# Kernel tuning notes

Hardware: AMD Instinct MI355X
Metric: run time of the kernel (lower is better)

The kernel has to match this reference:

```python
import jax, jax.numpy as jnp
import numpy as np

COV_EMB = 32
N_HEAD = 2
FACTOR_TCL = 2   # TemporalConvolutionalLayer factor (default 2)
FACTOR_MLP = 1   # MLP factor passed from MultiAttention init
EPS = 1e-5


def _conv1d_causal(x, w, b):
    # x: [N, C, T], w: [O, C, 3]; torch pads 2 both sides then slices [..., :-2],
    # equivalent to left-pad 2 only -> output length T.
    y = jax.lax.conv_general_dilated(x, w, window_strides=(1,), padding=[(2, 0)],
                                     dimension_numbers=('NCH', 'OIH', 'NCH'))
    return y + b[None, :, None]


def _tcl(x, w_conv, b_conv, w_proj, b_proj):
    # TemporalConvolutionalLayer: x [..., T, C] -> [..., T, C]
    shp = x.shape
    T, C = shp[-2], shp[-1]
    x2 = x.reshape(-1, T, C).transpose(0, 2, 1)              # [N, C, T]
    h = jax.nn.gelu(_conv1d_causal(x2, w_conv, b_conv), approximate=False)
    h = h.transpose(0, 2, 1)                                  # [N, T, 2C]
    out = h @ w_proj.T + b_proj                               # [N, T, C]
    return out.reshape(*shp[:-1], C)


def _layernorm(x, w):
    mu = jnp.mean(x, axis=-1, keepdims=True)
    var = jnp.var(x, axis=-1, keepdims=True)
    return (x - mu) * jax.lax.rsqrt(var + EPS) * w


def setup_inputs() -> dict:
    key = jax.random.key(0)
    ks = jax.random.split(key, 20)
    C = COV_EMB
    C2 = FACTOR_TCL * C
    s = 0.02
    inp = {
        'causal_decoder': jax.random.normal(ks[0], (8, 4, 1024, C), jnp.float32),
        'past_kv': jax.random.normal(ks[1], (8, 1024, C), jnp.float32),
    }
    def tcl_params(i):
        return (jax.random.normal(ks[i], (C2, C, 3), jnp.float32) * s,
                jnp.zeros((C2,), jnp.float32),
                jax.random.normal(ks[i + 1], (C, C2), jnp.float32) * s,
                jnp.zeros((C,), jnp.float32))
    inp['wq_conv'], inp['bq_conv'], inp['wq_proj'], inp['bq_proj'] = tcl_params(2)
    inp['wk_conv'], inp['bk_conv'], inp['wk_proj'], inp['bk_proj'] = tcl_params(4)
    inp['wv_conv'], inp['bv_conv'], inp['wv_proj'], inp['bv_proj'] = tcl_params(6)
    inp['w_cproj'] = jax.random.normal(ks[8], (C, C), jnp.float32) * s   # bias=False
    inp['ln_w'] = jnp.ones((C,), jnp.float32)                            # bias=False
    inp['w_fc'] = jax.random.normal(ks[9], (FACTOR_MLP * C, C), jnp.float32) * s   # bias=False
    inp['w_mlp_proj'] = jax.random.normal(ks[10], (C, FACTOR_MLP * C), jnp.float32) * s
    return inp


def reference(causal_decoder, past_kv,
              wq_conv, bq_conv, wq_proj, bq_proj,
              wk_conv, bk_conv, wk_proj, bk_proj,
              wv_conv, bv_conv, wv_proj, bv_proj,
              w_cproj, ln_w, w_fc, w_mlp_proj):
    B, F, T, C = causal_decoder.shape
    nh, hd = N_HEAD, C // N_HEAD

    q = _tcl(causal_decoder, wq_conv, bq_conv, wq_proj, bq_proj)   # [B,F,T,C]
    k = _tcl(past_kv, wk_conv, bk_conv, wk_proj, bk_proj)          # [B,S,C]
    v = _tcl(past_kv, wv_conv, bv_conv, wv_proj, bv_proj)          # [B,S,C]

    S = k.shape[1]
    q = q.reshape(B, F, T, nh, hd).transpose(0, 1, 3, 2, 4)        # [B,F,h,T,d]
    k = k.reshape(B, S, nh, hd).transpose(0, 2, 1, 3)              # [B,h,S,d]
    v = v.reshape(B, S, nh, hd).transpose(0, 2, 1, 3)              # [B,h,S,d]

    scale = 1.0 / jnp.sqrt(jnp.asarray(hd, q.dtype))
    scores = jnp.einsum('bfhtd,bhsd->bfhts', q, k) * scale          # [B,F,h,T,S]
    attn = jax.nn.softmax(scores, axis=-1)
    y = jnp.einsum('bfhts,bhsd->bfhtd', attn, v)                    # [B,F,h,T,d]
    y = y.transpose(0, 1, 3, 2, 4).reshape(B, F, T, C)

    out = causal_decoder + y @ w_cproj.T                            # resid_dropout = id (p=0)
    h = _layernorm(out, ln_w)
    mlp = jax.nn.gelu(h @ w_fc.T, approximate=False) @ w_mlp_proj.T
    out = out + mlp
    return out
```

## Files before the change

kernel.cpp:

```cpp
#include <hip/hip_runtime.h>

#define T_LEN 1024

typedef __attribute__((ext_vector_type(8))) short short8;
typedef __attribute__((ext_vector_type(4))) short short4v;
typedef __attribute__((ext_vector_type(4))) float float4v;

__device__ __forceinline__ float gelu_exact(float x) {
    return 0.5f * x * (1.0f + erff(x * 0.70710678118654752440f));
}
__device__ __forceinline__ unsigned short f2bf(float f) {
    unsigned u = __float_as_uint(f);
    u += 0x7fffu + ((u >> 16) & 1u);
    return (unsigned short)(u >> 16);
}

__global__ __launch_bounds__(256) void tcl_mfma(
    const float* __restrict__ cd, const float* __restrict__ pkv,
    const float* __restrict__ wqc, const float* __restrict__ bqc,
    const float* __restrict__ wqp, const float* __restrict__ bqp,
    const float* __restrict__ wkc, const float* __restrict__ bkc,
    const float* __restrict__ wkp, const float* __restrict__ bkp,
    const float* __restrict__ wvc, const float* __restrict__ bvc,
    const float* __restrict__ wvp, const float* __restrict__ bvp,
    unsigned short* __restrict__ qbf, unsigned short* __restrict__ kbf,
    unsigned short* __restrict__ vtbf)
{
    __shared__ __align__(16) unsigned short Abuf[32 * 96];
    __shared__ __align__(16) unsigned short WbT[64 * 96];
    __shared__ __align__(16) unsigned short Hb[32 * 72];
    __shared__ __align__(16) unsigned short WpB[32 * 72];

    const int tid = threadIdx.x;
    const int gb = blockIdx.x;

    const float *src, *wc, *bc, *wp, *bp;
    unsigned short* outb;
    int n, mode;
    if (gb < 1024)      { n = gb >> 5;           src = cd;  wc = wqc; bc = bqc; wp = wqp; bp = bqp; outb = qbf;  mode = 0; }
    else if (gb < 1280) { n = (gb - 1024) >> 5;  src = pkv; wc = wkc; bc = bkc; wp = wkp; bp = bkp; outb = kbf;  mode = 0; }
    else                { n = (gb - 1280) >> 5;  src = pkv; wc = wvc; bc = bvc; wp = wvp; bp = bvp; outb = vtbf; mode = 1; }
    const int t0 = (gb & 31) * 32;

#pragma unroll
    for (int it = 0; it < 3; ++it) {
        int s = (tid + it * 256) >> 3;
        int sub = tid & 7;
        int t = s / 3, tap = s - t * 3;
        int tau = t0 + t - 2 + tap;
        float4 xv = make_float4(0.f, 0.f, 0.f, 0.f);
        if (tau >= 0) xv = *(const float4*)&src[((size_t)n * T_LEN + tau) * 32 + sub * 4];
        short4v pk = { (short)f2bf(xv.x), (short)f2bf(xv.y),
                       (short)f2bf(xv.z), (short)f2bf(xv.w) };
        *(short4v*)&Abuf[t * 96 + tap * 32 + sub * 4] = pk;
    }
#pragma unroll
    for (int it = 0; it < 6; ++it) {
        int i4 = tid + it * 256;
        int idx = i4 * 4;
        int o = idx / 96, r = idx - o * 96;
        float4 w4 = *(const float4*)&wc[idx];
        float we[4] = { w4.x, w4.y, w4.z, w4.w };
#pragma unroll
        for (int e = 0; e < 4; ++e) {
            int re = r + e, c = re / 3, tap = re - c * 3;
            WbT[o * 96 + tap * 32 + c] = f2bf(we[e]);
        }
    }
#pragma unroll
    for (int it = 0; it < 2; ++it) {
        int i4 = tid + it * 256;
        int idx = i4 * 4;
        int c = idx >> 6, o = idx & 63;
        float4 w4 = *(const float4*)&wp[idx];
        short4v pk = { (short)f2bf(w4.x), (short)f2bf(w4.y),
                       (short)f2bf(w4.z), (short)f2bf(w4.w) };
        *(short4v*)&WpB[c * 72 + o] = pk;
    }

    const int w = tid >> 6;
    const int ln = tid & 63;
    const int sn = ln & 15;
    const int quad = ln >> 4;

    const float bcv = bc[w * 16 + sn];
    const int tmw = w & 1, cnw = w >> 1;
    const float bpv = bp[cnw * 16 + sn];

    __syncthreads();

    short8 b0 = *(const short8*)&WbT[(w * 16 + sn) * 96 + 0  + quad * 8];
    short8 b1 = *(const short8*)&WbT[(w * 16 + sn) * 96 + 32 + quad * 8];
    short8 b2 = *(const short8*)&WbT[(w * 16 + sn) * 96 + 64 + quad * 8];
    float4v zero = { 0.f, 0.f, 0.f, 0.f };
    float4v acc[2] = { zero, zero };
#pragma unroll
    for (int tm = 0; tm < 2; ++tm) {
        const unsigned short* ar = &Abuf[(tm * 16 + sn) * 96 + quad * 8];
        short8 a0 = *(const short8*)(ar + 0);
        short8 a1 = *(const short8*)(ar + 32);
        short8 a2 = *(const short8*)(ar + 64);
        acc[tm] = __builtin_amdgcn_mfma_f32_16x16x32_bf16(a0, b0, acc[tm], 0, 0, 0);
        acc[tm] = __builtin_amdgcn_mfma_f32_16x16x32_bf16(a1, b1, acc[tm], 0, 0, 0);
        acc[tm] = __builtin_amdgcn_mfma_f32_16x16x32_bf16(a2, b2, acc[tm], 0, 0, 0);
    }
#pragma unroll
    for (int tm = 0; tm < 2; ++tm) {
        float ge[4];
        ge[0] = gelu_exact(acc[tm].x + bcv);
        ge[1] = gelu_exact(acc[tm].y + bcv);
        ge[2] = gelu_exact(acc[tm].z + bcv);
        ge[3] = gelu_exact(acc[tm].w + bcv);
#pragma unroll
        for (int i = 0; i < 4; ++i)
            Hb[(tm * 16 + quad * 4 + i) * 72 + w * 16 + sn] = f2bf(ge[i]);
    }

    __syncthreads();

    const unsigned short* hr = &Hb[(tmw * 16 + sn) * 72 + quad * 8];
    short8 pa0 = *(const short8*)(hr + 0);
    short8 pa1 = *(const short8*)(hr + 32);
    short8 pb0 = *(const short8*)&WpB[(cnw * 16 + sn) * 72 + quad * 8];
    short8 pb1 = *(const short8*)&WpB[(cnw * 16 + sn) * 72 + 32 + quad * 8];
    float4v pacc = zero;
    pacc = __builtin_amdgcn_mfma_f32_16x16x32_bf16(pa0, pb0, pacc, 0, 0, 0);
    pacc = __builtin_amdgcn_mfma_f32_16x16x32_bf16(pa1, pb1, pacc, 0, 0, 0);

    float v[4] = { pacc.x + bpv, pacc.y + bpv, pacc.z + bpv, pacc.w + bpv };
#pragma unroll
    for (int i = 0; i < 4; ++i) {
        int t = tmw * 16 + quad * 4 + i;
        int c = cnw * 16 + sn;
        if (mode == 0) {
            outb[((size_t)n * T_LEN + t0 + t) * 32 + c] = f2bf(v[i]);
        } else {
            outb[((size_t)(n * 2 + cnw) * 16 + sn) * T_LEN + t0 + t] = f2bf(v[i]);
        }
    }
}

__global__ __launch_bounds__(256) void attn_kernel(
    const unsigned short* __restrict__ qbf,
    const unsigned short* __restrict__ kbf,
    const unsigned short* __restrict__ vtbf,
    float* __restrict__ yws)
{
    __shared__ unsigned short plds[4 * 2 * 16 * 36];

    const int tid = threadIdx.x;
    const int w = tid >> 6;
    const int ln = tid & 63;
    const int sn = ln & 15;
    const int quad = ln >> 4;
    const int g = blockIdx.x;
    const int tt = g & 15;
    const int bfh = g >> 4;
    const int h = bfh & 1;
    const int bf = bfh >> 1;
    const int b = bf >> 2;
    const int trow = tt * 64 + w * 16 + sn;

    short8 aq = {0, 0, 0, 0, 0, 0, 0, 0};
    if (quad < 2)
        aq = *(const short8*)(qbf + ((size_t)bf * T_LEN + trow) * 32 + h * 16 + quad * 8);

    const unsigned short* kb = kbf + (size_t)b * T_LEN * 32 + h * 16 + quad * 8;
    const unsigned short* vb = vtbf + ((size_t)(b * 2 + h) * 16 + sn) * T_LEN + quad * 8;
    unsigned short* pwA = plds + w * 1152;
    unsigned short* pwB = pwA + 576;

    float4v yacc = {0.f, 0.f, 0.f, 0.f};
    float l0 = 0.f, l1 = 0.f, l2 = 0.f, l3 = 0.f;
    const float SC = 0.36067376022224085f;

#pragma unroll 1
    for (int s0 = 0; s0 < 1024; s0 += 64) {
        short8 ka0 = {0,0,0,0,0,0,0,0}, ka1 = ka0, kb0 = ka0, kb1 = ka0;
        if (quad < 2) {
            ka0 = *(const short8*)(kb + (size_t)(s0 + sn) * 32);
            ka1 = *(const short8*)(kb + (size_t)(s0 + 16 + sn) * 32);
            kb0 = *(const short8*)(kb + (size_t)(s0 + 32 + sn) * 32);
            kb1 = *(const short8*)(kb + (size_t)(s0 + 48 + sn) * 32);
        }
        short8 bvA = *(const short8*)(vb + s0);
        short8 bvB = *(const short8*)(vb + s0 + 32);

        float4v z = {0.f, 0.f, 0.f, 0.f};
        float4v cA0 = __builtin_amdgcn_mfma_f32_16x16x32_bf16(aq, ka0, z, 0, 0, 0);
        float4v cA1 = __builtin_amdgcn_mfma_f32_16x16x32_bf16(aq, ka1, z, 0, 0, 0);
        float4v cB0 = __builtin_amdgcn_mfma_f32_16x16x32_bf16(aq, kb0, z, 0, 0, 0);
        float4v cB1 = __builtin_amdgcn_mfma_f32_16x16x32_bf16(aq, kb1, z, 0, 0, 0);

        float pA00 = exp2f(cA0.x * SC), pA01 = exp2f(cA0.y * SC);
        float pA02 = exp2f(cA0.z * SC), pA03 = exp2f(cA0.w * SC);
        float pA10 = exp2f(cA1.x * SC), pA11 = exp2f(cA1.y * SC);
        float pA12 = exp2f(cA1.z * SC), pA13 = exp2f(cA1.w * SC);
        float pB00 = exp2f(cB0.x * SC), pB01 = exp2f(cB0.y * SC);
        float pB02 = exp2f(cB0.z * SC), pB03 = exp2f(cB0.w * SC);
        float pB10 = exp2f(cB1.x * SC), pB11 = exp2f(cB1.y * SC);
        float pB12 = exp2f(cB1.z * SC), pB13 = exp2f(cB1.w * SC);

        l0 += (pA00 + pA10) + (pB00 + pB10);
        l1 += (pA01 + pA11) + (pB01 + pB11);
        l2 += (pA02 + pA12) + (pB02 + pB12);
        l3 += (pA03 + pA13) + (pB03 + pB13);

        const int tb = quad * 4;
        pwA[(tb + 0) * 36 + sn]      = f2bf(pA00);
        pwA[(tb + 1) * 36 + sn]      = f2bf(pA01);
        pwA[(tb + 2) * 36 + sn]      = f2bf(pA02);
        pwA[(tb + 3) * 36 + sn]      = f2bf(pA03);
        pwA[(tb + 0) * 36 + 16 + sn] = f2bf(pA10);
        pwA[(tb + 1) * 36 + 16 + sn] = f2bf(pA11);
        pwA[(tb + 2) * 36 + 16 + sn] = f2bf(pA12);
        pwA[(tb + 3) * 36 + 16 + sn] = f2bf(pA13);
        pwB[(tb + 0) * 36 + sn]      = f2bf(pB00);
        pwB[(tb + 1) * 36 + sn]      = f2bf(pB01);
        pwB[(tb + 2) * 36 + sn]      = f2bf(pB02);
        pwB[(tb + 3) * 36 + sn]      = f2bf(pB03);
        pwB[(tb + 0) * 36 + 16 + sn] = f2bf(pB10);
        pwB[(tb + 1) * 36 + 16 + sn] = f2bf(pB11);
        pwB[(tb + 2) * 36 + 16 + sn] = f2bf(pB12);
        pwB[(tb + 3) * 36 + 16 + sn] = f2bf(pB13);

        const unsigned short* prA = pwA + sn * 36 + quad * 8;
        const unsigned short* prB = pwB + sn * 36 + quad * 8;
        short4v aloA = *(const short4v*)prA;
        short4v ahiA = *(const short4v*)(prA + 4);
        short4v aloB = *(const short4v*)prB;
        short4v ahiB = *(const short4v*)(prB + 4);
        short8 apA = {aloA.x, aloA.y, aloA.z, aloA.w, ahiA.x, ahiA.y, ahiA.z, ahiA.w};
        short8 apB = {aloB.x, aloB.y, aloB.z, aloB.w, ahiB.x, ahiB.y, ahiB.z, ahiB.w};

        yacc = __builtin_amdgcn_mfma_f32_16x16x32_bf16(apA, bvA, yacc, 0, 0, 0);
        yacc = __builtin_amdgcn_mfma_f32_16x16x32_bf16(apB, bvB, yacc, 0, 0, 0);
    }

#pragma unroll
    for (int off = 1; off < 16; off <<= 1) {
        l0 += __shfl_xor(l0, off); l1 += __shfl_xor(l1, off);
        l2 += __shfl_xor(l2, off); l3 += __shfl_xor(l3, off);
    }
    const float i0 = 1.f / l0, i1 = 1.f / l1, i2 = 1.f / l2, i3 = 1.f / l3;

    float* yp = yws + ((size_t)bf * T_LEN + tt * 64 + w * 16 + quad * 4) * 32 + h * 16 + sn;
    yp[0 * 32] = yacc.x * i0;
    yp[1 * 32] = yacc.y * i1;
    yp[2 * 32] = yacc.z * i2;
    yp[3 * 32] = yacc.w * i3;
}

__global__ __launch_bounds__(256) void epi_kernel(
    const float* __restrict__ cd, const float* __restrict__ yws,
    const float* __restrict__ wcp, const float* __restrict__ lnw,
    const float* __restrict__ wfc, const float* __restrict__ wmp,
    float* __restrict__ out)
{
    __shared__ float sy[64][32];
    __shared__ float shn[8][36], sg[8][36];
    __shared__ float sln[32];

    const int tid = threadIdx.x;
    const int rl = tid >> 5, c = tid & 31;

    float wa[32], wb[32], wm[32];
#pragma unroll
    for (int j4 = 0; j4 < 8; ++j4) {
        float4 a = *(const float4*)(wcp + c * 32 + j4 * 4);
        wa[j4 * 4 + 0] = a.x; wa[j4 * 4 + 1] = a.y; wa[j4 * 4 + 2] = a.z; wa[j4 * 4 + 3] = a.w;
        float4 f = *(const float4*)(wfc + c * 32 + j4 * 4);
        wb[j4 * 4 + 0] = f.x; wb[j4 * 4 + 1] = f.y; wb[j4 * 4 + 2] = f.z; wb[j4 * 4 + 3] = f.w;
        float4 m = *(const float4*)(wmp + c * 32 + j4 * 4);
        wm[j4 * 4 + 0] = m.x; wm[j4 * 4 + 1] = m.y; wm[j4 * 4 + 2] = m.z; wm[j4 * 4 + 3] = m.w;
    }
    if (tid < 32) sln[tid] = lnw[tid];

    const size_t base = (size_t)blockIdx.x * 64;
    {
        const float4* ysrc = (const float4*)(yws + base * 32);
        float4* ydst = (float4*)&sy[0][0];
        for (int i = tid; i < 512; i += 256) ydst[i] = ysrc[i];
    }
    __syncthreads();
    const float lnwc = sln[c];

#pragma unroll 1
    for (int p = 0; p < 8; ++p) {
        int r = p * 8 + rl;
        size_t row = base + r;
        float x1 = cd[row * 32 + c];
#pragma unroll
        for (int j4 = 0; j4 < 8; ++j4) {
            float4 yv = *(const float4*)&sy[r][j4 * 4];
            x1 += wa[j4 * 4 + 0] * yv.x + wa[j4 * 4 + 1] * yv.y +
                  wa[j4 * 4 + 2] * yv.z + wa[j4 * 4 + 3] * yv.w;
        }
        float s1 = x1, s2 = x1 * x1;
#pragma unroll
        for (int off = 16; off; off >>= 1) {
            s1 += __shfl_xor(s1, off);
            s2 += __shfl_xor(s2, off);
        }
        float mu = s1 * (1.0f / 32.0f);
        float var = s2 * (1.0f / 32.0f) - mu * mu;
        float hn = (x1 - mu) * rsqrtf(var + 1e-5f) * lnwc;
        shn[rl][c] = hn;
        float ga = 0.f;
#pragma unroll
        for (int j4 = 0; j4 < 8; ++j4) {
            float4 hv = *(const float4*)&shn[rl][j4 * 4];
            ga += wb[j4 * 4 + 0] * hv.x + wb[j4 * 4 + 1] * hv.y +
                  wb[j4 * 4 + 2] * hv.z + wb[j4 * 4 + 3] * hv.w;
        }
        float gv = gelu_exact(ga);
        sg[rl][c] = gv;
        float oa = x1;
#pragma unroll
        for (int j4 = 0; j4 < 8; ++j4) {
            float4 gvv = *(const float4*)&sg[rl][j4 * 4];
            oa += wm[j4 * 4 + 0] * gvv.x + wm[j4 * 4 + 1] * gvv.y +
                  wm[j4 * 4 + 2] * gvv.z + wm[j4 * 4 + 3] * gvv.w;
        }
        out[row * 32 + c] = oa;
    }
}

extern "C" void kernel_launch(void* const* d_in, const int* in_sizes, int n_in,
                              void* d_out, int out_size, void* d_ws, size_t ws_size,
                              hipStream_t stream) {
    const float* cd  = (const float*)d_in[0];
    const float* pkv = (const float*)d_in[1];
    const float* wqc = (const float*)d_in[2];
    const float* bqc = (const float*)d_in[3];
    const float* wqp = (const float*)d_in[4];
    const float* bqp = (const float*)d_in[5];
    const float* wkc = (const float*)d_in[6];
    const float* bkc = (const float*)d_in[7];
    const float* wkp = (const float*)d_in[8];
    const float* bkp = (const float*)d_in[9];
    const float* wvc = (const float*)d_in[10];
    const float* bvc = (const float*)d_in[11];
    const float* wvp = (const float*)d_in[12];
    const float* bvp = (const float*)d_in[13];
    const float* wcp = (const float*)d_in[14];
    const float* lnw = (const float*)d_in[15];
    const float* wfc = (const float*)d_in[16];
    const float* wmp = (const float*)d_in[17];

    unsigned short* qbf  = (unsigned short*)d_ws;
    unsigned short* kbf  = qbf + (size_t)32 * 1024 * 32;
    unsigned short* vtbf = kbf + (size_t)8 * 1024 * 32;
    float* yws = (float*)(vtbf + (size_t)8 * 1024 * 32);

    tcl_mfma<<<1536, 256, 0, stream>>>(cd, pkv,
                                       wqc, bqc, wqp, bqp,
                                       wkc, bkc, wkp, bkp,
                                       wvc, bvc, wvp, bvp,
                                       qbf, kbf, vtbf);
    attn_kernel<<<1024, 256, 0, stream>>>(qbf, kbf, vtbf, yws);
    epi_kernel<<<512, 256, 0, stream>>>(cd, yws, wcp, lnw, wfc, wmp, (float*)d_out);
}
```

Measured before the change: 143.9 us.

## Fuse Q projection, attention and epilogue into one kernel; split out KV TCL

The Q temporal conv and projection, the attention, and the cproj/LayerNorm/MLP epilogue now run in a single 512-thread kernel per 64-row tile. Q and the attention output stay in shared memory instead of going through global workspace, and one launch is removed. K/V TCL stays in its own smaller kernel. In exchange each block uses about 62KB of LDS and 512 threads, which lowers occupancy. Epilogue weights move from registers to padded shared memory.

```diff
diff --git a/kernel.cpp b/kernel.cpp
--- a/kernel.cpp
+++ b/kernel.cpp
@@ -15,16 +15,13 @@
     return (unsigned short)(u >> 16);
 }
 
-__global__ __launch_bounds__(256) void tcl_mfma(
-    const float* __restrict__ cd, const float* __restrict__ pkv,
-    const float* __restrict__ wqc, const float* __restrict__ bqc,
-    const float* __restrict__ wqp, const float* __restrict__ bqp,
+__global__ __launch_bounds__(256) void kv_tcl(
+    const float* __restrict__ pkv,
     const float* __restrict__ wkc, const float* __restrict__ bkc,
     const float* __restrict__ wkp, const float* __restrict__ bkp,
     const float* __restrict__ wvc, const float* __restrict__ bvc,
     const float* __restrict__ wvp, const float* __restrict__ bvp,
-    unsigned short* __restrict__ qbf, unsigned short* __restrict__ kbf,
-    unsigned short* __restrict__ vtbf)
+    unsigned short* __restrict__ kbf, unsigned short* __restrict__ vtbf)
 {
     __shared__ __align__(16) unsigned short Abuf[32 * 96];
     __shared__ __align__(16) unsigned short WbT[64 * 96];
@@ -34,12 +31,11 @@
     const int tid = threadIdx.x;
     const int gb = blockIdx.x;
 
-    const float *src, *wc, *bc, *wp, *bp;
+    const float *wc, *bc, *wp, *bp;
     unsigned short* outb;
     int n, mode;
-    if (gb < 1024)      { n = gb >> 5;           src = cd;  wc = wqc; bc = bqc; wp = wqp; bp = bqp; outb = qbf;  mode = 0; }
-    else if (gb < 1280) { n = (gb - 1024) >> 5;  src = pkv; wc = wkc; bc = bkc; wp = wkp; bp = bkp; outb = kbf;  mode = 0; }
-    else                { n = (gb - 1280) >> 5;  src = pkv; wc = wvc; bc = bvc; wp = wvp; bp = bvp; outb = vtbf; mode = 1; }
+    if (gb < 256) { n = gb >> 5;         wc = wkc; bc = bkc; wp = wkp; bp = bkp; outb = kbf;  mode = 0; }
+    else          { n = (gb - 256) >> 5; wc = wvc; bc = bvc; wp = wvp; bp = bvp; outb = vtbf; mode = 1; }
     const int t0 = (gb & 31) * 32;
 
 #pragma unroll
@@ -49,7 +45,7 @@
         int t = s / 3, tap = s - t * 3;
         int tau = t0 + t - 2 + tap;
         float4 xv = make_float4(0.f, 0.f, 0.f, 0.f);
-        if (tau >= 0) xv = *(const float4*)&src[((size_t)n * T_LEN + tau) * 32 + sub * 4];
+        if (tau >= 0) xv = *(const float4*)&pkv[((size_t)n * T_LEN + tau) * 32 + sub * 4];
         short4v pk = { (short)f2bf(xv.x), (short)f2bf(xv.y),
                        (short)f2bf(xv.z), (short)f2bf(xv.w) };
         *(short4v*)&Abuf[t * 96 + tap * 32 + sub * 4] = pk;
@@ -140,37 +136,132 @@
     }
 }
 
-__global__ __launch_bounds__(256) void attn_kernel(
-    const unsigned short* __restrict__ qbf,
+__global__ __launch_bounds__(512) void fused_qae(
+    const float* __restrict__ cd,
+    const float* __restrict__ wqc, const float* __restrict__ bqc,
+    const float* __restrict__ wqp, const float* __restrict__ bqp,
     const unsigned short* __restrict__ kbf,
     const unsigned short* __restrict__ vtbf,
-    float* __restrict__ yws)
+    const float* __restrict__ wcp, const float* __restrict__ lnw,
+    const float* __restrict__ wfc, const float* __restrict__ wmp,
+    float* __restrict__ out)
 {
-    __shared__ unsigned short plds[4 * 2 * 16 * 36];
+    __shared__ __align__(16) char smem[61952];
+    unsigned short* Abuf = (unsigned short*)(smem);
+    unsigned short* WbT  = (unsigned short*)(smem + 12288);
+    unsigned short* Hb   = (unsigned short*)(smem + 24576);
+    unsigned short* WpB  = (unsigned short*)(smem + 33792);
+    unsigned short* qs   = (unsigned short*)(smem + 38400);
+    unsigned short* plds = (unsigned short*)(smem + 43520);
 
     const int tid = threadIdx.x;
+    const int bf = blockIdx.x >> 4;
+    const int tt = blockIdx.x & 15;
+    const int t0 = tt * 64;
+    const int b = bf >> 2;
+
+#pragma unroll
+    for (int it = 0; it < 3; ++it) {
+        int idx = tid + it * 512;
+        int s = idx >> 3;
+        int sub = idx & 7;
+        int t = s / 3, tap = s - t * 3;
+        int tau = t0 + t - 2 + tap;
+        float4 xv = make_float4(0.f, 0.f, 0.f, 0.f);
+        if (tau >= 0) xv = *(const float4*)&cd[((size_t)bf * T_LEN + tau) * 32 + sub * 4];
+        short4v pk = { (short)f2bf(xv.x), (short)f2bf(xv.y),
+                       (short)f2bf(xv.z), (short)f2bf(xv.w) };
+        *(short4v*)&Abuf[t * 96 + tap * 32 + sub * 4] = pk;
+    }
+#pragma unroll
+    for (int it = 0; it < 3; ++it) {
+        int i4 = tid + it * 512;
+        int idx = i4 * 4;
+        int o = idx / 96, r = idx - o * 96;
+        float4 w4 = *(const float4*)&wqc[idx];
+        float we[4] = { w4.x, w4.y, w4.z, w4.w };
+#pragma unroll
+        for (int e = 0; e < 4; ++e) {
+            int re = r + e, c = re / 3, tap = re - c * 3;
+            WbT[o * 96 + tap * 32 + c] = f2bf(we[e]);
+        }
+    }
+    {
+        int idx = tid * 4;
+        int c = idx >> 6, o = idx & 63;
+        float4 w4 = *(const float4*)&wqp[idx];
+        short4v pk = { (short)f2bf(w4.x), (short)f2bf(w4.y),
+                       (short)f2bf(w4.z), (short)f2bf(w4.w) };
+        *(short4v*)&WpB[c * 72 + o] = pk;
+    }
+
     const int w = tid >> 6;
     const int ln = tid & 63;
     const int sn = ln & 15;
     const int quad = ln >> 4;
-    const int g = blockIdx.x;
-    const int tt = g & 15;
-    const int bfh = g >> 4;
-    const int h = bfh & 1;
-    const int bf = bfh >> 1;
-    const int b = bf >> 2;
-    const int trow = tt * 64 + w * 16 + sn;
-
+    const float4v zero = { 0.f, 0.f, 0.f, 0.f };
+
+    __syncthreads();
+
+    {
+        const int tm = w & 3;
+        const int on0 = w >> 2, on1 = on0 + 2;
+        const unsigned short* ar = &Abuf[(tm * 16 + sn) * 96 + quad * 8];
+        short8 a0 = *(const short8*)(ar + 0);
+        short8 a1 = *(const short8*)(ar + 32);
+        short8 a2 = *(const short8*)(ar + 64);
+        const unsigned short* br0 = &WbT[(on0 * 16 + sn) * 96 + quad * 8];
+        const unsigned short* br1 = &WbT[(on1 * 16 + sn) * 96 + quad * 8];
+        float4v c0 = zero, c1 = zero;
+        c0 = __builtin_amdgcn_mfma_f32_16x16x32_bf16(a0, *(const short8*)(br0 + 0),  c0, 0, 0, 0);
+        c0 = __builtin_amdgcn_mfma_f32_16x16x32_bf16(a1, *(const short8*)(br0 + 32), c0, 0, 0, 0);
+        c0 = __builtin_amdgcn_mfma_f32_16x16x32_bf16(a2, *(const short8*)(br0 + 64), c0, 0, 0, 0);
+        c1 = __builtin_amdgcn_mfma_f32_16x16x32_bf16(a0, *(const short8*)(br1 + 0),  c1, 0, 0, 0);
+        c1 = __builtin_amdgcn_mfma_f32_16x16x32_bf16(a1, *(const short8*)(br1 + 32), c1, 0, 0, 0);
+        c1 = __builtin_amdgcn_mfma_f32_16x16x32_bf16(a2, *(const short8*)(br1 + 64), c1, 0, 0, 0);
+        const float bc0 = bqc[on0 * 16 + sn], bc1 = bqc[on1 * 16 + sn];
+        float g0[4] = { gelu_exact(c0.x + bc0), gelu_exact(c0.y + bc0),
+                        gelu_exact(c0.z + bc0), gelu_exact(c0.w + bc0) };
+        float g1[4] = { gelu_exact(c1.x + bc1), gelu_exact(c1.y + bc1),
+                        gelu_exact(c1.z + bc1), gelu_exact(c1.w + bc1) };
+#pragma unroll
+        for (int i = 0; i < 4; ++i) {
+            Hb[(tm * 16 + quad * 4 + i) * 72 + on0 * 16 + sn] = f2bf(g0[i]);
+            Hb[(tm * 16 + quad * 4 + i) * 72 + on1 * 16 + sn] = f2bf(g1[i]);
+        }
+    }
+    __syncthreads();
+
+    {
+        const int tm = w & 3, cn = w >> 2;
+        const unsigned short* hr = &Hb[(tm * 16 + sn) * 72 + quad * 8];
+        short8 pa0 = *(const short8*)(hr + 0);
+        short8 pa1 = *(const short8*)(hr + 32);
+        const unsigned short* wr_ = &WpB[(cn * 16 + sn) * 72 + quad * 8];
+        short8 pb0 = *(const short8*)(wr_ + 0);
+        short8 pb1 = *(const short8*)(wr_ + 32);
+        float4v pacc = zero;
+        pacc = __builtin_amdgcn_mfma_f32_16x16x32_bf16(pa0, pb0, pacc, 0, 0, 0);
+        pacc = __builtin_amdgcn_mfma_f32_16x16x32_bf16(pa1, pb1, pacc, 0, 0, 0);
+        const float bpv = bqp[cn * 16 + sn];
+        float v[4] = { pacc.x + bpv, pacc.y + bpv, pacc.z + bpv, pacc.w + bpv };
+#pragma unroll
+        for (int i = 0; i < 4; ++i)
+            qs[(tm * 16 + quad * 4 + i) * 40 + cn * 16 + sn] = f2bf(v[i]);
+    }
+    __syncthreads();
+
+    const int h = w & 1, rt = w >> 1;
     short8 aq = {0, 0, 0, 0, 0, 0, 0, 0};
     if (quad < 2)
-        aq = *(const short8*)(qbf + ((size_t)bf * T_LEN + trow) * 32 + h * 16 + quad * 8);
+        aq = *(const short8*)&qs[(rt * 16 + sn) * 40 + h * 16 + quad * 8];
 
     const unsigned short* kb = kbf + (size_t)b * T_LEN * 32 + h * 16 + quad * 8;
     const unsigned short* vb = vtbf + ((size_t)(b * 2 + h) * 16 + sn) * T_LEN + quad * 8;
     unsigned short* pwA = plds + w * 1152;
     unsigned short* pwB = pwA + 576;
 
-    float4v yacc = {0.f, 0.f, 0.f, 0.f};
+    float4v yacc = zero;
     float l0 = 0.f, l1 = 0.f, l2 = 0.f, l3 = 0.f;
     const float SC = 0.36067376022224085f;
 
@@ -186,11 +277,10 @@
         short8 bvA = *(const short8*)(vb + s0);
         short8 bvB = *(const short8*)(vb + s0 + 32);
 
-        float4v z = {0.f, 0.f, 0.f, 0.f};
-        float4v cA0 = __builtin_amdgcn_mfma_f32_16x16x32_bf16(aq, ka0, z, 0, 0, 0);
-        float4v cA1 = __builtin_amdgcn_mfma_f32_16x16x32_bf16(aq, ka1, z, 0, 0, 0);
-        float4v cB0 = __builtin_amdgcn_mfma_f32_16x16x32_bf16(aq, kb0, z, 0, 0, 0);
-        float4v cB1 = __builtin_amdgcn_mfma_f32_16x16x32_bf16(aq, kb1, z, 0, 0, 0);
+        float4v cA0 = __builtin_amdgcn_mfma_f32_16x16x32_bf16(aq, ka0, zero, 0, 0, 0);
+        float4v cA1 = __builtin_amdgcn_mfma_f32_16x16x32_bf16(aq, ka1, zero, 0, 0, 0);
+        float4v cB0 = __builtin_amdgcn_mfma_f32_16x16x32_bf16(aq, kb0, zero, 0, 0, 0);
+        float4v cB1 = __builtin_amdgcn_mfma_f32_16x16x32_bf16(aq, kb1, zero, 0, 0, 0);
 
         float pA00 = exp2f(cA0.x * SC), pA01 = exp2f(cA0.y * SC);
         float pA02 = exp2f(cA0.z * SC), pA03 = exp2f(cA0.w * SC);
@@ -242,59 +332,45 @@
         l0 += __shfl_xor(l0, off); l1 += __shfl_xor(l1, off);
         l2 += __shfl_xor(l2, off); l3 += __shfl_xor(l3, off);
     }
-    const float i0 = 1.f / l0, i1 = 1.f / l1, i2 = 1.f / l2, i3 = 1.f / l3;
-
-    float* yp = yws + ((size_t)bf * T_LEN + tt * 64 + w * 16 + quad * 4) * 32 + h * 16 + sn;
-    yp[0 * 32] = yacc.x * i0;
-    yp[1 * 32] = yacc.y * i1;
-    yp[2 * 32] = yacc.z * i2;
-    yp[3 * 32] = yacc.w * i3;
-}
-
-__global__ __launch_bounds__(256) void epi_kernel(
-    const float* __restrict__ cd, const float* __restrict__ yws,
-    const float* __restrict__ wcp, const float* __restrict__ lnw,
-    const float* __restrict__ wfc, const float* __restrict__ wmp,
-    float* __restrict__ out)
-{
-    __shared__ float sy[64][32];
-    __shared__ float shn[8][36], sg[8][36];
-    __shared__ float sln[32];
-
-    const int tid = threadIdx.x;
+
+    float* sy = (float*)smem;
+    {
+        const float i0 = 1.f / l0, i1 = 1.f / l1, i2 = 1.f / l2, i3 = 1.f / l3;
+        const int r0 = rt * 16 + quad * 4;
+        sy[(r0 + 0) * 32 + h * 16 + sn] = yacc.x * i0;
+        sy[(r0 + 1) * 32 + h * 16 + sn] = yacc.y * i1;
+        sy[(r0 + 2) * 32 + h * 16 + sn] = yacc.z * i2;
+        sy[(r0 + 3) * 32 + h * 16 + sn] = yacc.w * i3;
+    }
+    __syncthreads();
+
+    float* swc = (float*)(smem + 8192);
+    float* swf = (float*)(smem + 12800);
+    float* swm = (float*)(smem + 17408);
+    float* sln = (float*)(smem + 22016);
+    float* shn = (float*)(smem + 22144);
+    float* sgv = (float*)(smem + 24448);
+    for (int i = tid; i < 1024; i += 512) {
+        int r = i >> 5, cc = i & 31;
+        swc[r * 36 + cc] = wcp[i];
+        swf[r * 36 + cc] = wfc[i];
+        swm[r * 36 + cc] = wmp[i];
+    }
+    if (tid < 32) sln[tid] = lnw[tid];
+    __syncthreads();
+
     const int rl = tid >> 5, c = tid & 31;
-
-    float wa[32], wb[32], wm[32];
-#pragma unroll
-    for (int j4 = 0; j4 < 8; ++j4) {
-        float4 a = *(const float4*)(wcp + c * 32 + j4 * 4);
-        wa[j4 * 4 + 0] = a.x; wa[j4 * 4 + 1] = a.y; wa[j4 * 4 + 2] = a.z; wa[j4 * 4 + 3] = a.w;
-        float4 f = *(const float4*)(wfc + c * 32 + j4 * 4);
-        wb[j4 * 4 + 0] = f.x; wb[j4 * 4 + 1] = f.y; wb[j4 * 4 + 2] = f.z; wb[j4 * 4 + 3] = f.w;
-        float4 m = *(const float4*)(wmp + c * 32 + j4 * 4);
-        wm[j4 * 4 + 0] = m.x; wm[j4 * 4 + 1] = m.y; wm[j4 * 4 + 2] = m.z; wm[j4 * 4 + 3] = m.w;
-    }
-    if (tid < 32) sln[tid] = lnw[tid];
-
-    const size_t base = (size_t)blockIdx.x * 64;
-    {
-        const float4* ysrc = (const float4*)(yws + base * 32);
-        float4* ydst = (float4*)&sy[0][0];
-        for (int i = tid; i < 512; i += 256) ydst[i] = ysrc[i];
-    }
-    __syncthreads();
     const float lnwc = sln[c];
-
 #pragma unroll 1
-    for (int p = 0; p < 8; ++p) {
-        int r = p * 8 + rl;
-        size_t row = base + r;
+    for (int p = 0; p < 4; ++p) {
+        int r = p * 16 + rl;
+        size_t row = (size_t)bf * T_LEN + t0 + r;
         float x1 = cd[row * 32 + c];
 #pragma unroll
         for (int j4 = 0; j4 < 8; ++j4) {
-            float4 yv = *(const float4*)&sy[r][j4 * 4];
-            x1 += wa[j4 * 4 + 0] * yv.x + wa[j4 * 4 + 1] * yv.y +
-                  wa[j4 * 4 + 2] * yv.z + wa[j4 * 4 + 3] * yv.w;
+            float4 yv = *(const float4*)&sy[r * 32 + j4 * 4];
+            const float* wv = &swc[c * 36 + j4 * 4];
+            x1 += wv[0] * yv.x + wv[1] * yv.y + wv[2] * yv.z + wv[3] * yv.w;
         }
         float s1 = x1, s2 = x1 * x1;
 #pragma unroll
@@ -305,22 +381,22 @@
         float mu = s1 * (1.0f / 32.0f);
         float var = s2 * (1.0f / 32.0f) - mu * mu;
         float hn = (x1 - mu) * rsqrtf(var + 1e-5f) * lnwc;
-        shn[rl][c] = hn;
+        shn[rl * 36 + c] = hn;
         float ga = 0.f;
 #pragma unroll
         for (int j4 = 0; j4 < 8; ++j4) {
-            float4 hv = *(const float4*)&shn[rl][j4 * 4];
-            ga += wb[j4 * 4 + 0] * hv.x + wb[j4 * 4 + 1] * hv.y +
-                  wb[j4 * 4 + 2] * hv.z + wb[j4 * 4 + 3] * hv.w;
+            float4 hv = *(const float4*)&shn[rl * 36 + j4 * 4];
+            const float* wv = &swf[c * 36 + j4 * 4];
+            ga += wv[0] * hv.x + wv[1] * hv.y + wv[2] * hv.z + wv[3] * hv.w;
         }
         float gv = gelu_exact(ga);
-        sg[rl][c] = gv;
+        sgv[rl * 36 + c] = gv;
         float oa = x1;
 #pragma unroll
         for (int j4 = 0; j4 < 8; ++j4) {
-            float4 gvv = *(const float4*)&sg[rl][j4 * 4];
-            oa += wm[j4 * 4 + 0] * gvv.x + wm[j4 * 4 + 1] * gvv.y +
-                  wm[j4 * 4 + 2] * gvv.z + wm[j4 * 4 + 3] * gvv.w;
+            float4 gvv = *(const float4*)&sgv[rl * 36 + j4 * 4];
+            const float* wv = &swm[c * 36 + j4 * 4];
+            oa += wv[0] * gvv.x + wv[1] * gvv.y + wv[2] * gvv.z + wv[3] * gvv.w;
         }
         out[row * 32 + c] = oa;
     }
@@ -348,16 +424,11 @@
     const float* wfc = (const float*)d_in[16];
     const float* wmp = (const float*)d_in[17];
 
-    unsigned short* qbf  = (unsigned short*)d_ws;
-    unsigned short* kbf  = qbf + (size_t)32 * 1024 * 32;
+    unsigned short* kbf  = (unsigned short*)d_ws;
     unsigned short* vtbf = kbf + (size_t)8 * 1024 * 32;
-    float* yws = (float*)(vtbf + (size_t)8 * 1024 * 32);
-
-    tcl_mfma<<<1536, 256, 0, stream>>>(cd, pkv,
-                                       wqc, bqc, wqp, bqp,
-                                       wkc, bkc, wkp, bkp,
-                                       wvc, bvc, wvp, bvp,
-                                       qbf, kbf, vtbf);
-    attn_kernel<<<1024, 256, 0, stream>>>(qbf, kbf, vtbf, yws);
-    epi_kernel<<<512, 256, 0, stream>>>(cd, yws, wcp, lnw, wfc, wmp, (float*)d_out);
+
+    kv_tcl<<<512, 256, 0, stream>>>(pkv, wkc, bkc, wkp, bkp,
+                                    wvc, bvc, wvp, bvp, kbf, vtbf);
+    fused_qae<<<512, 512, 0, stream>>>(cd, wqc, bqc, wqp, bqp, kbf, vtbf,
+                                       wcp, lnw, wfc, wmp, (float*)d_out);
 }
```

Result: faster. 132.2 us (-8.1%).
